# Kernel tuning notes

Hardware: AMD Instinct MI355X
Metric: run time of the kernel (lower is better)

## Reference

```python
import jax, jax.numpy as jnp
import numpy as np

B, S, D, H = 2, 2048, 768, 12
HD = D // H


def setup_inputs() -> dict:
    key = jax.random.key(0)
    ks = jax.random.split(key, 6)
    sc = 1.0 / np.sqrt(D)
    return {
        "x": jax.random.normal(ks[0], (B, S, D), dtype=jnp.float32),
        "mask": jnp.tril(jnp.ones((S, S), dtype=jnp.int32)),  # causal GPT mask
        "Wq": jax.random.normal(ks[1], (D, D), dtype=jnp.float32) * sc,
        "bq": jnp.zeros((D,), dtype=jnp.float32),
        "Wk": jax.random.normal(ks[2], (D, D), dtype=jnp.float32) * sc,
        "bk": jnp.zeros((D,), dtype=jnp.float32),
        "Wv": jax.random.normal(ks[3], (D, D), dtype=jnp.float32) * sc,
        "bv": jnp.zeros((D,), dtype=jnp.float32),
        "Wo": jax.random.normal(ks[4], (D, D), dtype=jnp.float32) * sc,
        "bo": jnp.zeros((D,), dtype=jnp.float32),
    }


def reference(x, mask, Wq, bq, Wk, bk, Wv, bv, Wo, bo):
    # Linear projections (torch Linear: x @ W.T + b; here W stored as [in,out])
    Q = (x @ Wq + bq).reshape(B, S, H, HD).transpose(0, 2, 1, 3)  # [B,H,S,HD]
    K = (x @ Wk + bk).reshape(B, S, H, HD).transpose(0, 2, 1, 3)
    V = (x @ Wv + bv).reshape(B, S, H, HD).transpose(0, 2, 1, 3)

    scores = jnp.einsum('bhqd,bhkd->bhqk', Q, K) / jnp.sqrt(jnp.float32(HD))
    scores = jnp.where(mask[None, None, :, :] == 0, jnp.float32(-1e9), scores)
    attn_weights = jax.nn.softmax(scores, axis=-1)  # dropout is identity in eval
    attn_out = jnp.einsum('bhqk,bhkd->bhqd', attn_weights, V)

    attn_out = attn_out.transpose(0, 2, 1, 3).reshape(B, S, D)
    out = attn_out @ Wo + bo
    return out, attn_weights
```

## Files before the change

kernel.cpp:

```cpp
#include <hip/hip_runtime.h>

#define DEV static __device__ __forceinline__

typedef __bf16 bf16x8 __attribute__((ext_vector_type(8)));
typedef float  f32x4  __attribute__((ext_vector_type(4)));

DEV bf16x8 ld8(const __bf16* p) { return *reinterpret_cast<const bf16x8*>(p); }

DEV f32x4 mfma16(bf16x8 a, bf16x8 b, f32x4 c) {
  return __builtin_amdgcn_mfma_f32_16x16x32_bf16(a, b, c, 0, 0, 0);
}

#define SEQ 2048
#define DIM 768
#define NH  12
#define HDIM 64

DEV void decode_chunk(int cid, int CH, int& qt, int& t0) {
  int q = 0, rem = cid;
  while (true) {
    int nc = (q + CH) / CH;
    if (rem < nc) break;
    rem -= nc; ++q;
  }
  qt = q; t0 = rem * CH;
}

__global__ __launch_bounds__(256) void prep_wt(
    const float* __restrict__ Wq, const float* __restrict__ Wk,
    const float* __restrict__ Wv, const float* __restrict__ Wo,
    __bf16* __restrict__ WbT) {
  __shared__ float T[64][65];
  const int z = blockIdx.z;
  const float* W = (z == 0) ? Wq : (z == 1) ? Wk : (z == 2) ? Wv : Wo;
  const int kb = blockIdx.x * 64, nb = blockIdx.y * 64;
  const int t = threadIdx.x, r = t >> 2, c4 = (t & 3) * 16;
  #pragma unroll
  for (int j = 0; j < 16; j += 4) {
    f32x4 v = *(const f32x4*)(W + (size_t)(kb + r) * DIM + nb + c4 + j);
    T[r][c4 + j]     = v[0]; T[r][c4 + j + 1] = v[1];
    T[r][c4 + j + 2] = v[2]; T[r][c4 + j + 3] = v[3];
  }
  __syncthreads();
  bf16x8 o0, o1;
  #pragma unroll
  for (int j = 0; j < 8; ++j) {
    o0[j] = (__bf16)T[c4 + j][r];
    o1[j] = (__bf16)T[c4 + 8 + j][r];
  }
  __bf16* dst = WbT + (size_t)z * DIM * DIM + (size_t)(nb + r) * DIM + kb + c4;
  *(bf16x8*)dst = o0;
  *(bf16x8*)(dst + 8) = o1;
}

DEV void gemm_tile(const float* __restrict__ Af, const __bf16* __restrict__ Bt,
                   const float* __restrict__ bias, void* __restrict__ outp,
                   const int mode, const float scale,
                   const int mbase, const int nbase) {
  __shared__ __bf16 As[64][72];
  __shared__ __bf16 Bs[64][72];

  const int tid  = threadIdx.x;
  const int l    = tid & 63;
  const int w    = tid >> 6;
  const int lrow = l & 15;
  const int lk8  = (l >> 4) * 8;
  const int wrow = (w >> 1) * 32, wcol = (w & 1) * 32;

  f32x4 acc[2][2] = {};

  const int arow = tid >> 2;
  const int acol = (tid & 3) * 16;

  for (int kk = 0; kk < DIM; kk += 64) {
    {
      const float* src = Af + (size_t)(mbase + arow) * DIM + kk + acol;
      f32x4 f0 = *(const f32x4*)(src);
      f32x4 f1 = *(const f32x4*)(src + 4);
      f32x4 f2 = *(const f32x4*)(src + 8);
      f32x4 f3 = *(const f32x4*)(src + 12);
      bf16x8 v0, v1;
      #pragma unroll
      for (int j = 0; j < 4; ++j) {
        v0[j] = (__bf16)f0[j]; v0[4 + j] = (__bf16)f1[j];
        v1[j] = (__bf16)f2[j]; v1[4 + j] = (__bf16)f3[j];
      }
      *(bf16x8*)&As[arow][acol]     = v0;
      *(bf16x8*)&As[arow][acol + 8] = v1;
    }
    {
      const __bf16* bsrc = Bt + (size_t)(nbase + arow) * DIM + kk + acol;
      *(bf16x8*)&Bs[arow][acol]     = ld8(bsrc);
      *(bf16x8*)&Bs[arow][acol + 8] = ld8(bsrc + 8);
    }
    __syncthreads();
    #pragma unroll
    for (int kc = 0; kc < 2; ++kc) {
      bf16x8 a0 = ld8(&As[wrow + lrow][kc * 32 + lk8]);
      bf16x8 a1 = ld8(&As[wrow + 16 + lrow][kc * 32 + lk8]);
      bf16x8 b0 = ld8(&Bs[wcol + lrow][kc * 32 + lk8]);
      bf16x8 b1 = ld8(&Bs[wcol + 16 + lrow][kc * 32 + lk8]);
      acc[0][0] = mfma16(a0, b0, acc[0][0]);
      acc[0][1] = mfma16(a0, b1, acc[0][1]);
      acc[1][0] = mfma16(a1, b0, acc[1][0]);
      acc[1][1] = mfma16(a1, b1, acc[1][1]);
    }
    __syncthreads();
  }

  #pragma unroll
  for (int mi = 0; mi < 2; ++mi)
  #pragma unroll
  for (int ni = 0; ni < 2; ++ni) {
    const int n  = nbase + wcol + ni * 16 + lrow;
    const float bn = bias[n];
    const int hh = n >> 6, hd = n & 63;
    #pragma unroll
    for (int r = 0; r < 4; ++r) {
      const int m = mbase + wrow + mi * 16 + (l >> 4) * 4 + r;
      const float v = (acc[mi][ni][r] + bn) * scale;
      const int bb = m >> 11, s = m & (SEQ - 1);
      if (mode == 0) {
        ((__bf16*)outp)[(((size_t)(bb * NH + hh) * SEQ) + s) * HDIM + hd] = (__bf16)v;
      } else if (mode == 1) {
        ((__bf16*)outp)[(((size_t)(bb * NH + hh) * HDIM) + hd) * SEQ + s] = (__bf16)v;
      } else {
        ((float*)outp)[(size_t)m * DIM + n] = v;
      }
    }
  }
}

__global__ __launch_bounds__(256, 4) void qkv_gemm(
    const float* __restrict__ x, const __bf16* __restrict__ WbT,
    const float* __restrict__ bq, const float* __restrict__ bk,
    const float* __restrict__ bv,
    __bf16* __restrict__ Qb, __bf16* __restrict__ Kb, __bf16* __restrict__ Vt) {
  const int z = blockIdx.z;
  const __bf16* Bt = WbT + (size_t)z * DIM * DIM;
  const float* bs = (z == 0) ? bq : (z == 1) ? bk : bv;
  void* o = (z == 0) ? (void*)Qb : (z == 1) ? (void*)Kb : (void*)Vt;
  const float sc = (z == 0) ? 0.125f : 1.f;
  gemm_tile(x, Bt, bs, o, (z == 2) ? 1 : 0, sc, blockIdx.y * 64, blockIdx.x * 64);
}

__global__ __launch_bounds__(256, 4) void out_gemm(
    const float* __restrict__ A, const __bf16* __restrict__ WbT,
    const float* __restrict__ bo, float* __restrict__ out) {
  gemm_tile(A, WbT + (size_t)3 * DIM * DIM, bo, out, 2, 1.f,
            blockIdx.y * 64, blockIdx.x * 64);
}

__global__ __launch_bounds__(256) void zero_f32(float* __restrict__ p, int n4) {
  const f32x4 zv = {0.f, 0.f, 0.f, 0.f};
  int i = blockIdx.x * 256 + threadIdx.x;
  const int stride = gridDim.x * 256;
  for (; i < n4; i += stride) ((f32x4*)p)[i] = zv;
}

__global__ __launch_bounds__(256, 4) void attn_sums(
    const __bf16* __restrict__ Q, const __bf16* __restrict__ K,
    float* __restrict__ sums, float* __restrict__ Wout) {
  const int tid = threadIdx.x, l = tid & 63, w = tid >> 6;
  const int lrow = l & 15, lk8 = (l >> 4) * 8, g = l >> 4;
  const int lin = blockIdx.x;
  const int C = 144;
  const int bh = (lin & 7) * 3 + (lin >> 3) / C;
  const int cid = (lin >> 3) % C;
  int qt, t0; decode_chunk(cid, 4, qt, t0);
  const int t1 = (t0 + 4 < qt + 1) ? t0 + 4 : qt + 1;
  const int qw = qt * 64 + w * 16;
  const int q  = qw + lrow;

  const __bf16* Qh = Q + (size_t)bh * SEQ * HDIM;
  const __bf16* Kh = K + (size_t)bh * SEQ * HDIM;
  const bf16x8 bq0 = ld8(Qh + (size_t)q * HDIM + lk8);
  const bf16x8 bq1 = ld8(Qh + (size_t)q * HDIM + 32 + lk8);

  float ssum = 0.f;
  for (int t = t0; t < t1; ++t) {
    const int kb = t * 64;
    #pragma unroll
    for (int nt = 0; nt < 4; ++nt) {
      const int krow = kb + nt * 16 + lrow;
      const bf16x8 ak0 = ld8(Kh + (size_t)krow * HDIM + lk8);
      const bf16x8 ak1 = ld8(Kh + (size_t)krow * HDIM + 32 + lk8);
      f32x4 s0 = {0.f, 0.f, 0.f, 0.f}, s1 = {0.f, 0.f, 0.f, 0.f};
      s0 = mfma16(ak0, bq0, s0);
      s1 = mfma16(ak1, bq1, s1);
      const int k0 = kb + nt * 16 + g * 4;
      if (t < qt || k0 + 3 <= q) {
        #pragma unroll
        for (int r = 0; r < 4; ++r) ssum += __expf(s0[r] + s1[r]);
      } else {
        #pragma unroll
        for (int r = 0; r < 4; ++r)
          ssum += (k0 + r <= q) ? __expf(s0[r] + s1[r]) : 0.f;
      }
    }
  }
  ssum += __shfl_xor(ssum, 16);
  ssum += __shfl_xor(ssum, 32);
  if (g == 0) unsafeAtomicAdd(&sums[bh * SEQ + q], ssum);

  const int tz = (t1 < qt) ? t1 : qt;
  if (t0 < tz) {
    float* Wg = Wout + (size_t)bh * SEQ * SEQ;
    const int zr = tid >> 2;
    const int zc = (tid & 3) * 4;
    const f32x4 zv = {0.f, 0.f, 0.f, 0.f};
    for (int t = t0; t < tz; ++t) {
      float* base = Wg + (size_t)(t * 64 + zr) * SEQ + qt * 64 + zc;
      #pragma unroll
      for (int c = 0; c < 4; ++c) *(f32x4*)(base + c * 16) = zv;
    }
  }
}

__global__ __launch_bounds__(256, 4) void attn_wpv(
    const __bf16* __restrict__ Q, const __bf16* __restrict__ K,
    const __bf16* __restrict__ VT, const float* __restrict__ sums,
    float* __restrict__ Wout, float* __restrict__ AOf) {
  __shared__ float Plds[4][16][68];

  const int tid = threadIdx.x, l = tid & 63, w = tid >> 6;
  const int lrow = l & 15, lk8 = (l >> 4) * 8, g = l >> 4;
  const int lin = blockIdx.x;
  const int C = 80;
  const int bh = (lin & 7) * 3 + (lin >> 3) / C;
  const int cid = (lin >> 3) % C;
  int qt, t0; decode_chunk(cid, 8, qt, t0);
  const int t1 = (t0 + 8 < qt + 1) ? t0 + 8 : qt + 1;
  const int bb = bh / NH, hh = bh % NH;
  const int qw = qt * 64 + w * 16;
  const int q  = qw + lrow;

  const __bf16* Qh = Q + (size_t)bh * SEQ * HDIM;
  const __bf16* Kh = K + (size_t)bh * SEQ * HDIM;
  const __bf16* Vh = VT + (size_t)bh * HDIM * SEQ;
  float* Wg = Wout + (size_t)bh * SEQ * SEQ;

  const bf16x8 bq0 = ld8(Qh + (size_t)q * HDIM + lk8);
  const bf16x8 bq1 = ld8(Qh + (size_t)q * HDIM + 32 + lk8);
  const float inv = 1.f / sums[bh * SEQ + q];

  f32x4 acco[4] = {};
  for (int t = t0; t < t1; ++t) {
    const int kb = t * 64;
    #pragma unroll
    for (int nt = 0; nt < 4; ++nt) {
      const int krow = kb + nt * 16 + lrow;
      const bf16x8 ak0 = ld8(Kh + (size_t)krow * HDIM + lk8);
      const bf16x8 ak1 = ld8(Kh + (size_t)krow * HDIM + 32 + lk8);
      f32x4 s0 = {0.f, 0.f, 0.f, 0.f}, s1 = {0.f, 0.f, 0.f, 0.f};
      s0 = mfma16(ak0, bq0, s0);
      s1 = mfma16(ak1, bq1, s1);
      const int k0 = kb + nt * 16 + g * 4;
      f32x4 pv;
      if (t < qt || k0 + 3 <= q) {
        #pragma unroll
        for (int r = 0; r < 4; ++r) pv[r] = __expf(s0[r] + s1[r]) * inv;
      } else {
        #pragma unroll
        for (int r = 0; r < 4; ++r)
          pv[r] = (k0 + r <= q) ? __expf(s0[r] + s1[r]) * inv : 0.f;
      }
      *(f32x4*)&Wg[(size_t)q * SEQ + k0] = pv;
      *(f32x4*)&Plds[w][lrow][nt * 16 + g * 4] = pv;
    }
    #pragma unroll
    for (int kc = 0; kc < 2; ++kc) {
      const float* ps = &Plds[w][lrow][kc * 32 + lk8];
      const f32x4 p0 = *(const f32x4*)ps;
      const f32x4 p1 = *(const f32x4*)(ps + 4);
      bf16x8 aw;
      #pragma unroll
      for (int j = 0; j < 4; ++j) { aw[j] = (__bf16)p0[j]; aw[4 + j] = (__bf16)p1[j]; }
      #pragma unroll
      for (int nt = 0; nt < 4; ++nt) {
        const bf16x8 bv =
            ld8(Vh + (size_t)(nt * 16 + lrow) * SEQ + kb + kc * 32 + lk8);
        acco[nt] = mfma16(aw, bv, acco[nt]);
      }
    }
  }

  #pragma unroll
  for (int nt = 0; nt < 4; ++nt)
    #pragma unroll
    for (int r = 0; r < 4; ++r)
      unsafeAtomicAdd(
          &AOf[(size_t)(bb * SEQ + qw + g * 4 + r) * DIM + hh * HDIM + nt * 16 + lrow],
          acco[nt][r]);
}

extern "C" void kernel_launch(void* const* d_in, const int* in_sizes, int n_in,
                              void* d_out, int out_size, void* d_ws, size_t ws_size,
                              hipStream_t stream) {
  const float* x  = (const float*)d_in[0];
  const float* Wq = (const float*)d_in[2];
  const float* bq = (const float*)d_in[3];
  const float* Wk = (const float*)d_in[4];
  const float* bk = (const float*)d_in[5];
  const float* Wv = (const float*)d_in[6];
  const float* bv = (const float*)d_in[7];
  const float* Wo = (const float*)d_in[8];
  const float* bo = (const float*)d_in[9];

  char* wsb = (char*)d_ws;
  __bf16* Qb   = (__bf16*)(wsb);
  __bf16* Kb   = (__bf16*)(wsb + 6291456);
  __bf16* Vt   = (__bf16*)(wsb + 12582912);
  float*  AOf  = (float*)(wsb + 18874368);
  float*  sums = (float*)(wsb + 31457280);
  __bf16* WbT  = (__bf16*)(wsb + 31653888);

  float* out   = (float*)d_out;
  float* attnW = out + 3145728;

  zero_f32<<<1024, 256, 0, stream>>>(AOf, (3145728 + 49152) / 4);
  prep_wt<<<dim3(12, 12, 4), 256, 0, stream>>>(Wq, Wk, Wv, Wo, WbT);
  qkv_gemm<<<dim3(12, 64, 3), 256, 0, stream>>>(x, WbT, bq, bk, bv, Qb, Kb, Vt);
  attn_sums<<<24 * 144, 256, 0, stream>>>(Qb, Kb, sums, attnW);
  attn_wpv<<<24 * 80, 256, 0, stream>>>(Qb, Kb, Vt, sums, attnW, AOf);
  out_gemm<<<dim3(12, 64), 256, 0, stream>>>(AOf, WbT, bo, out);
}
```

Measured before the change: 309.1 us.

## Process 128 query rows per block in attention and pre-convert x to bf16

The attention kernels now give each wave two 16-row query fragments, so one block covers 128 query rows. Each K and V fragment load is reused across twice as many queries, and causal chunk decoding is adjusted for the doubled tile. A separate kernel converts x to bf16 once, using the attention-weights output buffer as scratch before it is overwritten, so the QKV GEMM no longer re-converts fp32 tiles for each of its three projections. The larger tiles raise register and LDS pressure per block and halve the number of blocks, and the scratch reuse relies on kernel ordering.

New measurement: 279.8 us. 9.5% less time.

```diff
diff --git a/kernel.cpp b/kernel.cpp
--- a/kernel.cpp
+++ b/kernel.cpp
@@ -16,14 +16,25 @@
 #define NH  12
 #define HDIM 64
 
-DEV void decode_chunk(int cid, int CH, int& qt, int& t0) {
+DEV void decode_chunk2(int cid, int CH, int& qt, int& t0) {
   int q = 0, rem = cid;
   while (true) {
-    int nc = (q + CH) / CH;
+    int nc = (2 * q + 2 + CH - 1) / CH;
     if (rem < nc) break;
     rem -= nc; ++q;
   }
   qt = q; t0 = rem * CH;
+}
+
+__global__ __launch_bounds__(256) void cvt_x(const float* __restrict__ x,
+                                             __bf16* __restrict__ xb) {
+  const int i = (blockIdx.x * 256 + threadIdx.x) * 8;
+  f32x4 a = *(const f32x4*)(x + i);
+  f32x4 b = *(const f32x4*)(x + i + 4);
+  bf16x8 v;
+  #pragma unroll
+  for (int j = 0; j < 4; ++j) { v[j] = (__bf16)a[j]; v[4 + j] = (__bf16)b[j]; }
+  *(bf16x8*)(xb + i) = v;
 }
 
 __global__ __launch_bounds__(256) void prep_wt(
@@ -53,7 +64,8 @@
   *(bf16x8*)(dst + 8) = o1;
 }
 
-DEV void gemm_tile(const float* __restrict__ Af, const __bf16* __restrict__ Bt,
+DEV void gemm_tile(const float* __restrict__ Af, const __bf16* __restrict__ Ab,
+                   const __bf16* __restrict__ Bt,
                    const float* __restrict__ bias, void* __restrict__ outp,
                    const int mode, const float scale,
                    const int mbase, const int nbase) {
@@ -73,7 +85,11 @@
   const int acol = (tid & 3) * 16;
 
   for (int kk = 0; kk < DIM; kk += 64) {
-    {
+    if (Ab) {
+      const __bf16* asrc = Ab + (size_t)(mbase + arow) * DIM + kk + acol;
+      *(bf16x8*)&As[arow][acol]     = ld8(asrc);
+      *(bf16x8*)&As[arow][acol + 8] = ld8(asrc + 8);
+    } else {
       const float* src = Af + (size_t)(mbase + arow) * DIM + kk + acol;
       f32x4 f0 = *(const f32x4*)(src);
       f32x4 f1 = *(const f32x4*)(src + 4);
@@ -132,7 +148,7 @@
 }
 
 __global__ __launch_bounds__(256, 4) void qkv_gemm(
-    const float* __restrict__ x, const __bf16* __restrict__ WbT,
+    const __bf16* __restrict__ xb, const __bf16* __restrict__ WbT,
     const float* __restrict__ bq, const float* __restrict__ bk,
     const float* __restrict__ bv,
     __bf16* __restrict__ Qb, __bf16* __restrict__ Kb, __bf16* __restrict__ Vt) {
@@ -141,13 +157,14 @@
   const float* bs = (z == 0) ? bq : (z == 1) ? bk : bv;
   void* o = (z == 0) ? (void*)Qb : (z == 1) ? (void*)Kb : (void*)Vt;
   const float sc = (z == 0) ? 0.125f : 1.f;
-  gemm_tile(x, Bt, bs, o, (z == 2) ? 1 : 0, sc, blockIdx.y * 64, blockIdx.x * 64);
+  gemm_tile(nullptr, xb, Bt, bs, o, (z == 2) ? 1 : 0, sc,
+            blockIdx.y * 64, blockIdx.x * 64);
 }
 
 __global__ __launch_bounds__(256, 4) void out_gemm(
     const float* __restrict__ A, const __bf16* __restrict__ WbT,
     const float* __restrict__ bo, float* __restrict__ out) {
-  gemm_tile(A, WbT + (size_t)3 * DIM * DIM, bo, out, 2, 1.f,
+  gemm_tile(A, nullptr, WbT + (size_t)3 * DIM * DIM, bo, out, 2, 1.f,
             blockIdx.y * 64, blockIdx.x * 64);
 }
 
@@ -164,55 +181,80 @@
   const int tid = threadIdx.x, l = tid & 63, w = tid >> 6;
   const int lrow = l & 15, lk8 = (l >> 4) * 8, g = l >> 4;
   const int lin = blockIdx.x;
-  const int C = 144;
+  const int C = 72;
   const int bh = (lin & 7) * 3 + (lin >> 3) / C;
   const int cid = (lin >> 3) % C;
-  int qt, t0; decode_chunk(cid, 4, qt, t0);
-  const int t1 = (t0 + 4 < qt + 1) ? t0 + 4 : qt + 1;
-  const int qw = qt * 64 + w * 16;
-  const int q  = qw + lrow;
+  int qt, t0; decode_chunk2(cid, 4, qt, t0);
+  const int tmax = 2 * qt + 2;
+  const int t1 = (t0 + 4 < tmax) ? t0 + 4 : tmax;
+  const int fb0 = qt * 128 + w * 32;
+  const int fb1 = fb0 + 16;
+  const int q0 = fb0 + lrow, q1 = fb1 + lrow;
 
   const __bf16* Qh = Q + (size_t)bh * SEQ * HDIM;
   const __bf16* Kh = K + (size_t)bh * SEQ * HDIM;
-  const bf16x8 bq0 = ld8(Qh + (size_t)q * HDIM + lk8);
-  const bf16x8 bq1 = ld8(Qh + (size_t)q * HDIM + 32 + lk8);
-
-  float ssum = 0.f;
+  const bf16x8 bqA0 = ld8(Qh + (size_t)q0 * HDIM + lk8);
+  const bf16x8 bqA1 = ld8(Qh + (size_t)q0 * HDIM + 32 + lk8);
+  const bf16x8 bqB0 = ld8(Qh + (size_t)q1 * HDIM + lk8);
+  const bf16x8 bqB1 = ld8(Qh + (size_t)q1 * HDIM + 32 + lk8);
+
+  float sA = 0.f, sB = 0.f;
   for (int t = t0; t < t1; ++t) {
     const int kb = t * 64;
+    const bool liveA = (kb <= fb0 + 15);
+    const bool liveB = (kb <= fb1 + 15);
+    if (!liveB) continue;
     #pragma unroll
     for (int nt = 0; nt < 4; ++nt) {
       const int krow = kb + nt * 16 + lrow;
       const bf16x8 ak0 = ld8(Kh + (size_t)krow * HDIM + lk8);
       const bf16x8 ak1 = ld8(Kh + (size_t)krow * HDIM + 32 + lk8);
-      f32x4 s0 = {0.f, 0.f, 0.f, 0.f}, s1 = {0.f, 0.f, 0.f, 0.f};
-      s0 = mfma16(ak0, bq0, s0);
-      s1 = mfma16(ak1, bq1, s1);
       const int k0 = kb + nt * 16 + g * 4;
-      if (t < qt || k0 + 3 <= q) {
-        #pragma unroll
-        for (int r = 0; r < 4; ++r) ssum += __expf(s0[r] + s1[r]);
-      } else {
-        #pragma unroll
-        for (int r = 0; r < 4; ++r)
-          ssum += (k0 + r <= q) ? __expf(s0[r] + s1[r]) : 0.f;
-      }
-    }
-  }
-  ssum += __shfl_xor(ssum, 16);
-  ssum += __shfl_xor(ssum, 32);
-  if (g == 0) unsafeAtomicAdd(&sums[bh * SEQ + q], ssum);
-
-  const int tz = (t1 < qt) ? t1 : qt;
+      if (liveA) {
+        f32x4 s0 = {0.f, 0.f, 0.f, 0.f}, s1 = {0.f, 0.f, 0.f, 0.f};
+        s0 = mfma16(ak0, bqA0, s0);
+        s1 = mfma16(ak1, bqA1, s1);
+        if (kb + 63 <= fb0) {
+          #pragma unroll
+          for (int r = 0; r < 4; ++r) sA += __expf(s0[r] + s1[r]);
+        } else {
+          #pragma unroll
+          for (int r = 0; r < 4; ++r)
+            sA += (k0 + r <= q0) ? __expf(s0[r] + s1[r]) : 0.f;
+        }
+      }
+      {
+        f32x4 s0 = {0.f, 0.f, 0.f, 0.f}, s1 = {0.f, 0.f, 0.f, 0.f};
+        s0 = mfma16(ak0, bqB0, s0);
+        s1 = mfma16(ak1, bqB1, s1);
+        if (kb + 63 <= fb1) {
+          #pragma unroll
+          for (int r = 0; r < 4; ++r) sB += __expf(s0[r] + s1[r]);
+        } else {
+          #pragma unroll
+          for (int r = 0; r < 4; ++r)
+            sB += (k0 + r <= q1) ? __expf(s0[r] + s1[r]) : 0.f;
+        }
+      }
+    }
+  }
+  sA += __shfl_xor(sA, 16); sA += __shfl_xor(sA, 32);
+  sB += __shfl_xor(sB, 16); sB += __shfl_xor(sB, 32);
+  if (g == 0) {
+    unsafeAtomicAdd(&sums[bh * SEQ + q0], sA);
+    unsafeAtomicAdd(&sums[bh * SEQ + q1], sB);
+  }
+
+  const int tz = (t1 < 2 * qt) ? t1 : 2 * qt;
   if (t0 < tz) {
     float* Wg = Wout + (size_t)bh * SEQ * SEQ;
     const int zr = tid >> 2;
-    const int zc = (tid & 3) * 4;
+    const int zc = (tid & 3) * 32;
     const f32x4 zv = {0.f, 0.f, 0.f, 0.f};
     for (int t = t0; t < tz; ++t) {
-      float* base = Wg + (size_t)(t * 64 + zr) * SEQ + qt * 64 + zc;
+      float* base = Wg + (size_t)(t * 64 + zr) * SEQ + qt * 128 + zc;
       #pragma unroll
-      for (int c = 0; c < 4; ++c) *(f32x4*)(base + c * 16) = zv;
+      for (int c = 0; c < 8; ++c) *(f32x4*)(base + c * 4) = zv;
     }
   }
 }
@@ -221,66 +263,111 @@
     const __bf16* __restrict__ Q, const __bf16* __restrict__ K,
     const __bf16* __restrict__ VT, const float* __restrict__ sums,
     float* __restrict__ Wout, float* __restrict__ AOf) {
-  __shared__ float Plds[4][16][68];
+  __shared__ float Plds[4][2][16][68];
 
   const int tid = threadIdx.x, l = tid & 63, w = tid >> 6;
   const int lrow = l & 15, lk8 = (l >> 4) * 8, g = l >> 4;
   const int lin = blockIdx.x;
-  const int C = 80;
+  const int C = 40;
   const int bh = (lin & 7) * 3 + (lin >> 3) / C;
   const int cid = (lin >> 3) % C;
-  int qt, t0; decode_chunk(cid, 8, qt, t0);
-  const int t1 = (t0 + 8 < qt + 1) ? t0 + 8 : qt + 1;
+  int qt, t0; decode_chunk2(cid, 8, qt, t0);
+  const int tmax = 2 * qt + 2;
+  const int t1 = (t0 + 8 < tmax) ? t0 + 8 : tmax;
   const int bb = bh / NH, hh = bh % NH;
-  const int qw = qt * 64 + w * 16;
-  const int q  = qw + lrow;
+  const int fb0 = qt * 128 + w * 32;
+  const int fb1 = fb0 + 16;
+  const int q0 = fb0 + lrow, q1 = fb1 + lrow;
 
   const __bf16* Qh = Q + (size_t)bh * SEQ * HDIM;
   const __bf16* Kh = K + (size_t)bh * SEQ * HDIM;
   const __bf16* Vh = VT + (size_t)bh * HDIM * SEQ;
   float* Wg = Wout + (size_t)bh * SEQ * SEQ;
 
-  const bf16x8 bq0 = ld8(Qh + (size_t)q * HDIM + lk8);
-  const bf16x8 bq1 = ld8(Qh + (size_t)q * HDIM + 32 + lk8);
-  const float inv = 1.f / sums[bh * SEQ + q];
-
-  f32x4 acco[4] = {};
+  const bf16x8 bqA0 = ld8(Qh + (size_t)q0 * HDIM + lk8);
+  const bf16x8 bqA1 = ld8(Qh + (size_t)q0 * HDIM + 32 + lk8);
+  const bf16x8 bqB0 = ld8(Qh + (size_t)q1 * HDIM + lk8);
+  const bf16x8 bqB1 = ld8(Qh + (size_t)q1 * HDIM + 32 + lk8);
+  const float invA = 1.f / sums[bh * SEQ + q0];
+  const float invB = 1.f / sums[bh * SEQ + q1];
+
+  f32x4 accA[4] = {}, accB[4] = {};
   for (int t = t0; t < t1; ++t) {
     const int kb = t * 64;
+    const bool liveA = (kb <= fb0 + 15);
+    const bool liveB = (kb <= fb1 + 15);
+    const f32x4 zv = {0.f, 0.f, 0.f, 0.f};
+    if (!liveB) {
+      #pragma unroll
+      for (int nt = 0; nt < 4; ++nt) {
+        const int k0 = kb + nt * 16 + g * 4;
+        *(f32x4*)&Wg[(size_t)q0 * SEQ + k0] = zv;
+        *(f32x4*)&Wg[(size_t)q1 * SEQ + k0] = zv;
+      }
+      continue;
+    }
     #pragma unroll
     for (int nt = 0; nt < 4; ++nt) {
       const int krow = kb + nt * 16 + lrow;
       const bf16x8 ak0 = ld8(Kh + (size_t)krow * HDIM + lk8);
       const bf16x8 ak1 = ld8(Kh + (size_t)krow * HDIM + 32 + lk8);
-      f32x4 s0 = {0.f, 0.f, 0.f, 0.f}, s1 = {0.f, 0.f, 0.f, 0.f};
-      s0 = mfma16(ak0, bq0, s0);
-      s1 = mfma16(ak1, bq1, s1);
       const int k0 = kb + nt * 16 + g * 4;
-      f32x4 pv;
-      if (t < qt || k0 + 3 <= q) {
+      f32x4 pvA = zv;
+      if (liveA) {
+        f32x4 s0 = {0.f, 0.f, 0.f, 0.f}, s1 = {0.f, 0.f, 0.f, 0.f};
+        s0 = mfma16(ak0, bqA0, s0);
+        s1 = mfma16(ak1, bqA1, s1);
+        if (kb + 63 <= fb0) {
+          #pragma unroll
+          for (int r = 0; r < 4; ++r) pvA[r] = __expf(s0[r] + s1[r]) * invA;
+        } else {
+          #pragma unroll
+          for (int r = 0; r < 4; ++r)
+            pvA[r] = (k0 + r <= q0) ? __expf(s0[r] + s1[r]) * invA : 0.f;
+        }
+        *(f32x4*)&Plds[w][0][lrow][nt * 16 + g * 4] = pvA;
+      }
+      *(f32x4*)&Wg[(size_t)q0 * SEQ + k0] = pvA;
+      f32x4 pvB;
+      {
+        f32x4 s0 = {0.f, 0.f, 0.f, 0.f}, s1 = {0.f, 0.f, 0.f, 0.f};
+        s0 = mfma16(ak0, bqB0, s0);
+        s1 = mfma16(ak1, bqB1, s1);
+        if (kb + 63 <= fb1) {
+          #pragma unroll
+          for (int r = 0; r < 4; ++r) pvB[r] = __expf(s0[r] + s1[r]) * invB;
+        } else {
+          #pragma unroll
+          for (int r = 0; r < 4; ++r)
+            pvB[r] = (k0 + r <= q1) ? __expf(s0[r] + s1[r]) * invB : 0.f;
+        }
+      }
+      *(f32x4*)&Wg[(size_t)q1 * SEQ + k0] = pvB;
+      *(f32x4*)&Plds[w][1][lrow][nt * 16 + g * 4] = pvB;
+    }
+    #pragma unroll
+    for (int kc = 0; kc < 2; ++kc) {
+      bf16x8 awA, awB;
+      if (liveA) {
+        const float* ps = &Plds[w][0][lrow][kc * 32 + lk8];
+        const f32x4 p0 = *(const f32x4*)ps;
+        const f32x4 p1 = *(const f32x4*)(ps + 4);
         #pragma unroll
-        for (int r = 0; r < 4; ++r) pv[r] = __expf(s0[r] + s1[r]) * inv;
-      } else {
+        for (int j = 0; j < 4; ++j) { awA[j] = (__bf16)p0[j]; awA[4 + j] = (__bf16)p1[j]; }
+      }
+      {
+        const float* ps = &Plds[w][1][lrow][kc * 32 + lk8];
+        const f32x4 p0 = *(const f32x4*)ps;
+        const f32x4 p1 = *(const f32x4*)(ps + 4);
         #pragma unroll
-        for (int r = 0; r < 4; ++r)
-          pv[r] = (k0 + r <= q) ? __expf(s0[r] + s1[r]) * inv : 0.f;
-      }
-      *(f32x4*)&Wg[(size_t)q * SEQ + k0] = pv;
-      *(f32x4*)&Plds[w][lrow][nt * 16 + g * 4] = pv;
-    }
-    #pragma unroll
-    for (int kc = 0; kc < 2; ++kc) {
-      const float* ps = &Plds[w][lrow][kc * 32 + lk8];
-      const f32x4 p0 = *(const f32x4*)ps;
-      const f32x4 p1 = *(const f32x4*)(ps + 4);
-      bf16x8 aw;
-      #pragma unroll
-      for (int j = 0; j < 4; ++j) { aw[j] = (__bf16)p0[j]; aw[4 + j] = (__bf16)p1[j]; }
+        for (int j = 0; j < 4; ++j) { awB[j] = (__bf16)p0[j]; awB[4 + j] = (__bf16)p1[j]; }
+      }
       #pragma unroll
       for (int nt = 0; nt < 4; ++nt) {
         const bf16x8 bv =
             ld8(Vh + (size_t)(nt * 16 + lrow) * SEQ + kb + kc * 32 + lk8);
-        acco[nt] = mfma16(aw, bv, acco[nt]);
+        if (liveA) accA[nt] = mfma16(awA, bv, accA[nt]);
+        accB[nt] = mfma16(awB, bv, accB[nt]);
       }
     }
   }
@@ -288,10 +375,14 @@
   #pragma unroll
   for (int nt = 0; nt < 4; ++nt)
     #pragma unroll
-    for (int r = 0; r < 4; ++r)
+    for (int r = 0; r < 4; ++r) {
       unsafeAtomicAdd(
-          &AOf[(size_t)(bb * SEQ + qw + g * 4 + r) * DIM + hh * HDIM + nt * 16 + lrow],
-          acco[nt][r]);
+          &AOf[(size_t)(bb * SEQ + fb0 + g * 4 + r) * DIM + hh * HDIM + nt * 16 + lrow],
+          accA[nt][r]);
+      unsafeAtomicAdd(
+          &AOf[(size_t)(bb * SEQ + fb1 + g * 4 + r) * DIM + hh * HDIM + nt * 16 + lrow],
+          accB[nt][r]);
+    }
 }
 
 extern "C" void kernel_launch(void* const* d_in, const int* in_sizes, int n_in,
@@ -317,11 +408,13 @@
 
   float* out   = (float*)d_out;
   float* attnW = out + 3145728;
+  __bf16* xb   = (__bf16*)attnW;
 
   zero_f32<<<1024, 256, 0, stream>>>(AOf, (3145728 + 49152) / 4);
+  cvt_x<<<1536, 256, 0, stream>>>(x, xb);
   prep_wt<<<dim3(12, 12, 4), 256, 0, stream>>>(Wq, Wk, Wv, Wo, WbT);
-  qkv_gemm<<<dim3(12, 64, 3), 256, 0, stream>>>(x, WbT, bq, bk, bv, Qb, Kb, Vt);
-  attn_sums<<<24 * 144, 256, 0, stream>>>(Qb, Kb, sums, attnW);
-  attn_wpv<<<24 * 80, 256, 0, stream>>>(Qb, Kb, Vt, sums, attnW, AOf);
+  qkv_gemm<<<dim3(12, 64, 3), 256, 0, stream>>>(xb, WbT, bq, bk, bv, Qb, Kb, Vt);
+  attn_sums<<<1728, 256, 0, stream>>>(Qb, Kb, sums, attnW);
+  attn_wpv<<<960, 256, 0, stream>>>(Qb, Kb, Vt, sums, attnW, AOf);
   out_gemm<<<dim3(12, 64), 256, 0, stream>>>(AOf, WbT, bo, out);
 }
```
